# Kernel tuning notes

Hardware: AMD Instinct MI355X
Metric: run time of the kernel (lower is better)

The kernel has to match this reference:

```python
import jax, jax.numpy as jnp
import numpy as np

B, S, D = 2, 2048, 1024
H, DK, DV = 16, 64, 64
DFF = 4096
EPS_RMS = 1e-6


def setup_inputs() -> dict:
    key = jax.random.key(0)
    ks = jax.random.split(key, 10)
    sc = 0.02
    return {
        "x": jax.random.normal(ks[0], (B, S, D), jnp.float32),
        "w_q": jax.random.normal(ks[1], (D, H * DK), jnp.float32) * sc,
        "w_k": jax.random.normal(ks[2], (D, H * DK), jnp.float32) * sc,
        "w_v": jax.random.normal(ks[3], (D, H * DV), jnp.float32) * sc,
        "w_o": jax.random.normal(ks[4], (H * DV, D), jnp.float32) * sc,
        "w_gate": jax.random.normal(ks[5], (D, DFF), jnp.float32) * sc,
        "w_up": jax.random.normal(ks[6], (D, DFF), jnp.float32) * sc,
        "w_down": jax.random.normal(ks[7], (DFF, D), jnp.float32) * sc,
        "g1": jnp.ones((D,), jnp.float32),
        "g2": jnp.ones((D,), jnp.float32),
    }


def _rmsnorm(x, g):
    var = jnp.mean(jnp.square(x), axis=-1, keepdims=True)
    return x * jax.lax.rsqrt(var + EPS_RMS) * g


def _stable_softmax(s):
    # Faithful to source: exp(x) / (sum exp(x) + 1e-9); fully-masked rows -> 0.
    e = jnp.exp(s)
    return e / (jnp.sum(e, axis=-1, keepdims=True) + 1e-9)


def reference(x, w_q, w_k, w_v, w_o, w_gate, w_up, w_down, g1, g2):
    b, s, d = x.shape
    h = _rmsnorm(x, g1)
    q = (h @ w_q).reshape(b, s, H, DK).transpose(0, 2, 1, 3)  # [B,H,S,DK]
    k = (h @ w_k).reshape(b, s, H, DK).transpose(0, 2, 1, 3)
    v = (h @ w_v).reshape(b, s, H, DV).transpose(0, 2, 1, 3)
    scores = jnp.einsum("bhqd,bhkd->bhqk", q, k) / jnp.sqrt(jnp.asarray(DK, x.dtype))
    # triu with diagonal=0: self and future positions are masked
    mask = jnp.triu(jnp.ones((s, s), bool))
    scores = jnp.where(mask, -jnp.inf, scores)
    attn = _stable_softmax(scores)  # [B,H,S,S]
    av = jnp.einsum("bhqk,bhkd->bhqd", attn, v)
    av = av.transpose(0, 2, 1, 3).reshape(b, s, H * DV)
    x = x + av @ w_o  # residual 1
    h2 = _rmsnorm(x, g2)
    hidden = jax.nn.silu(h2 @ w_gate) * (h2 @ w_up)
    return x + hidden @ w_down  # residual 2
```

## Files before the change

### kernel.cpp

```cpp
#include <hip/hip_runtime.h>
#include <cstdint>
#include <cstddef>

typedef unsigned short u16;
typedef unsigned int u32;
typedef __bf16 bf16x8 __attribute__((ext_vector_type(8)));
typedef float floatx4 __attribute__((ext_vector_type(4)));
typedef float floatx16 __attribute__((ext_vector_type(16)));

#define B_ 2
#define S_ 2048
#define D_ 1024
#define H_ 16
#define DFF_ 4096
#define BS_ 4096

__device__ __forceinline__ u16 f2bf(float f) {
  u32 u = __builtin_bit_cast(u32, f);
  u += 0x7fffu + ((u >> 16) & 1u);
  return (u16)(u >> 16);
}
__device__ __forceinline__ float bf2f(u16 h) {
  u32 u = ((u32)h) << 16;
  return __builtin_bit_cast(float, u);
}

__device__ __forceinline__ void gl_lds16(const u16* g, u16* l) {
  __builtin_amdgcn_global_load_lds(
      (const __attribute__((address_space(1))) void*)g,
      (__attribute__((address_space(3))) void*)l, 16, 0, 0);
}

__global__ void prep_weights(const float* __restrict__ wq, const float* __restrict__ wk,
                             const float* __restrict__ wv, const float* __restrict__ wo,
                             const float* __restrict__ wg, const float* __restrict__ wu,
                             const float* __restrict__ wd,
                             u16* __restrict__ wqkv_t, u16* __restrict__ wo_t,
                             u16* __restrict__ wgu_t, u16* __restrict__ wdn_t) {
  __shared__ float tile[32][33];
  const int id = blockIdx.x;
  const float* src;
  u16* dst;
  int R, C, bx, by, mode;
  if (id < 3072) {
    const int which = id >> 10, lo = id & 1023;
    src = which == 0 ? wq : (which == 1 ? wk : wv);
    dst = wqkv_t + which * 1024 * 1024;
    R = 1024; C = 1024; bx = lo & 31; by = lo >> 5; mode = 0;
  } else if (id < 4096) {
    const int lo = id - 3072;
    src = wo; dst = wo_t; R = 1024; C = 1024; bx = lo & 31; by = lo >> 5; mode = 0;
  } else if (id < 8192) {
    const int lo = id - 4096;
    src = wg; dst = wgu_t; R = 1024; C = 4096; bx = lo & 127; by = lo >> 7; mode = 1;
  } else if (id < 12288) {
    const int lo = id - 8192;
    src = wu; dst = wgu_t; R = 1024; C = 4096; bx = lo & 127; by = lo >> 7; mode = 2;
  } else {
    const int lo = id - 12288;
    src = wd; dst = wdn_t; R = 4096; C = 1024; bx = lo & 31; by = lo >> 5; mode = 0;
  }
  const int tx = threadIdx.x, ty = threadIdx.y;
  const int c0 = bx * 32, r0 = by * 32;
#pragma unroll
  for (int i = 0; i < 4; i++)
    tile[ty + i * 8][tx] = src[(size_t)(r0 + ty + i * 8) * C + c0 + tx];
  __syncthreads();
#pragma unroll
  for (int i = 0; i < 4; i++) {
    const int oc = c0 + ty + i * 8;
    const int orow = (mode == 0) ? oc
                                 : ((oc >> 5) * 64 + (oc & 31) + (mode == 2 ? 32 : 0));
    dst[(size_t)orow * R + r0 + tx] = f2bf(tile[tx][ty + i * 8]);
  }
}

__global__ __launch_bounds__(256) void rmsnorm_kernel(const float* __restrict__ x,
                                                      const float* __restrict__ g,
                                                      u16* __restrict__ out) {
  const int row = blockIdx.x, t = threadIdx.x;
  const float4 v = ((const float4*)(x + (size_t)row * 1024))[t];
  float ss = v.x * v.x + v.y * v.y + v.z * v.z + v.w * v.w;
#pragma unroll
  for (int off = 32; off > 0; off >>= 1) ss += __shfl_xor(ss, off);
  __shared__ float red[4];
  if ((t & 63) == 0) red[t >> 6] = ss;
  __syncthreads();
  ss = red[0] + red[1] + red[2] + red[3];
  const float inv = rsqrtf(ss * (1.0f / 1024.0f) + 1e-6f);
  const float4 gv = ((const float4*)g)[t];
  uint2 o;
  o.x = (u32)f2bf(v.x * inv * gv.x) | ((u32)f2bf(v.y * inv * gv.y) << 16);
  o.y = (u32)f2bf(v.z * inv * gv.z) | ((u32)f2bf(v.w * inv * gv.w) << 16);
  ((uint2*)(out + (size_t)row * 1024))[t] = o;
}

__global__ __launch_bounds__(256) void vtrans_kernel(const u16* __restrict__ qkv,
                                                     u16* __restrict__ vT) {
  __shared__ u16 tile[64][72];
  const int t = threadIdx.x;
  const int s0 = blockIdx.x * 64, h = blockIdx.y, b = blockIdx.z;
  const int r = t >> 2, cc = t & 3;
  const u16* src = qkv + (size_t)(b * S_ + s0 + r) * 3072 + 2 * D_ + h * 64 + cc * 16;
  *(uint4*)(&tile[r][cc * 16]) = *(const uint4*)src;
  *(uint4*)(&tile[r][cc * 16 + 8]) = *(const uint4*)(src + 8);
  __syncthreads();
  union { uint4 u[2]; u16 s[16]; } o;
#pragma unroll
  for (int j = 0; j < 16; j++) o.s[j] = tile[cc * 16 + j][r];
  u16* dst = vT + (size_t)((b * H_ + h) * 64 + r) * S_ + s0 + cc * 16;
  *(uint4*)dst = o.u[0];
  *(uint4*)(dst + 8) = o.u[1];
}

template <int BN, int EPI>
__global__ __launch_bounds__(256) void gemm_bt(const u16* __restrict__ A,
                                               const u16* __restrict__ Bt,
                                               void* __restrict__ Cout,
                                               const float* __restrict__ res,
                                               int M, int N, int K) {
  __shared__ u16 As[128 * 64];
  __shared__ u16 Bs[BN * 64];
  constexpr int NTI = BN / 64;
  constexpr int NSEG = 16 + BN / 8;
  constexpr int SPW = NSEG / 4;
  const int t = threadIdx.x, w = t >> 6, l = t & 63;
  const int m0 = blockIdx.y * 128, n0 = blockIdx.x * BN;
  const int wm = w >> 1, wn = w & 1;
  const int c31 = l & 31, khalf = l >> 5;

  const u16* gsrc[SPW];
  u16* ldst[SPW];
  {
    const int rl = l >> 3, ch = (l & 7) ^ rl;
#pragma unroll
    for (int i = 0; i < SPW; i++) {
      const int s = w * SPW + i;
      if (s < 16) {
        gsrc[i] = A + (size_t)(m0 + s * 8 + rl) * K + ch * 8;
        ldst[i] = As + s * 512;
      } else {
        gsrc[i] = Bt + (size_t)(n0 + (s - 16) * 8 + rl) * K + ch * 8;
        ldst[i] = Bs + (s - 16) * 512;
      }
    }
  }

  floatx16 acc[2][NTI] = {};

  for (int kk = 0; kk < K; kk += 64) {
    __syncthreads();
#pragma unroll
    for (int i = 0; i < SPW; i++) gl_lds16(gsrc[i], ldst[i]);
#pragma unroll
    for (int i = 0; i < SPW; i++) gsrc[i] += 64;
    __syncthreads();

#pragma unroll
    for (int ks = 0; ks < 4; ks++) {
      bf16x8 af[2], bfr[NTI];
#pragma unroll
      for (int mi = 0; mi < 2; mi++) {
        const int row = wm * 64 + mi * 32 + c31;
        const int e = (ks * 2 + khalf) ^ (row & 7);
        af[mi] = *(const bf16x8*)(As + row * 64 + e * 8);
      }
#pragma unroll
      for (int ni = 0; ni < NTI; ni++) {
        const int row = wn * (BN / 2) + ni * 32 + c31;
        const int e = (ks * 2 + khalf) ^ (row & 7);
        bfr[ni] = *(const bf16x8*)(Bs + row * 64 + e * 8);
      }
#pragma unroll
      for (int mi = 0; mi < 2; mi++)
#pragma unroll
        for (int ni = 0; ni < NTI; ni++)
          acc[mi][ni] = __builtin_amdgcn_mfma_f32_32x32x16_bf16(af[mi], bfr[ni],
                                                                acc[mi][ni], 0, 0, 0);
    }
  }

  if (EPI == 2) {
#pragma unroll
    for (int mi = 0; mi < 2; mi++) {
      const int colo = ((int)blockIdx.x * 2 + wn) * 32 + c31;
#pragma unroll
      for (int reg = 0; reg < 16; reg++) {
        const int row = m0 + wm * 64 + mi * 32 + (reg & 3) + 8 * (reg >> 2) + 4 * khalf;
        const float g = acc[mi][0][reg];
        const float u = acc[mi][1][reg];
        ((u16*)Cout)[(size_t)row * 4096 + colo] = f2bf(g / (1.f + __expf(-g)) * u);
      }
    }
  } else {
#pragma unroll
    for (int mi = 0; mi < 2; mi++)
#pragma unroll
      for (int ni = 0; ni < NTI; ni++) {
        const int col = n0 + wn * (BN / 2) + ni * 32 + c31;
#pragma unroll
        for (int reg = 0; reg < 16; reg++) {
          const int row = m0 + wm * 64 + mi * 32 + (reg & 3) + 8 * (reg >> 2) + 4 * khalf;
          const size_t idx = (size_t)row * N + col;
          if (EPI == 0) ((u16*)Cout)[idx] = f2bf(acc[mi][ni][reg]);
          else          ((float*)Cout)[idx] = acc[mi][ni][reg] + res[idx];
        }
      }
  }
}

__global__ __launch_bounds__(256) void attn_kernel(const u16* __restrict__ qkv,
                                                   const u16* __restrict__ vT,
                                                   u16* __restrict__ av) {
  __shared__ u16 SM[2 * 8192];
  __shared__ u16 Ps[4 * 2048];
  const int t = threadIdx.x, w = t >> 6, l = t & 63;
  const int lrow = l & 15, lk = l >> 4;
  const int bh = blockIdx.x;
  const int b = bh >> 4, h = bh & 15;
  const int qt = 15 - (int)blockIdx.y;
  const int qbase = qt * 128 + w * 32;
  const int ktmax = 2 * qt + 1;
  u16* Pw = Ps + w * 2048;

  bf16x8 aq[2][2];
#pragma unroll
  for (int sub = 0; sub < 2; sub++)
#pragma unroll
    for (int half = 0; half < 2; half++)
      aq[sub][half] = *(const bf16x8*)(qkv + (size_t)(b * S_ + qbase + sub * 16 + lrow) * 3072 +
                                       h * 64 + half * 32 + lk * 8);

  const u16* gcur[4];
  int gstep[4], loff[4];
#pragma unroll
  for (int i = 0; i < 4; i++) {
    const int c = w + 4 * i;
    const int half = (c >> 2) & 1, grp = c & 3;
    if (c < 8) {
      gcur[i] = qkv + (size_t)(b * S_ + grp * 16 + (l >> 2)) * 3072 + D_ + h * 64 +
                half * 32 + (l & 3) * 8;
      gstep[i] = 64 * 3072;
      loff[i] = half * 2048 + grp * 512;
    } else {
      gcur[i] = vT + (size_t)(bh * 64 + grp * 16 + (l >> 2)) * S_ + half * 32 + (l & 3) * 8;
      gstep[i] = 64;
      loff[i] = 4096 + half * 2048 + grp * 512;
    }
  }

  floatx4 oacc[2][4] = {};
  float den[2][4] = {};

  int cur = 0;
#pragma unroll
  for (int i = 0; i < 4; i++) { gl_lds16(gcur[i], SM + loff[i]); gcur[i] += gstep[i]; }

  for (int kt = 0; kt <= ktmax; kt++) {
    __syncthreads();
    if (kt < ktmax) {
#pragma unroll
      for (int i = 0; i < 4; i++) {
        gl_lds16(gcur[i], SM + (cur ^ 1) * 8192 + loff[i]);
        gcur[i] += gstep[i];
      }
    }
    const u16* Kbuf = SM + cur * 8192;
    const u16* Vbuf = Kbuf + 4096;

    bf16x8 bk[4][2];
#pragma unroll
    for (int ct = 0; ct < 4; ct++)
#pragma unroll
      for (int half = 0; half < 2; half++)
        bk[ct][half] = *(const bf16x8*)(Kbuf + half * 2048 + (ct * 16 + lrow) * 32 + lk * 8);
    floatx4 sf[2][4] = {};
#pragma unroll
    for (int sub = 0; sub < 2; sub++)
#pragma unroll
      for (int ct = 0; ct < 4; ct++) {
        sf[sub][ct] = __builtin_amdgcn_mfma_f32_16x16x32_bf16(aq[sub][0], bk[ct][0],
                                                              sf[sub][ct], 0, 0, 0);
        sf[sub][ct] = __builtin_amdgcn_mfma_f32_16x16x32_bf16(aq[sub][1], bk[ct][1],
                                                              sf[sub][ct], 0, 0, 0);
      }

#pragma unroll
    for (int sub = 0; sub < 2; sub++)
#pragma unroll
      for (int ct = 0; ct < 4; ct++) {
        const int kpos = kt * 64 + ct * 16 + lrow;
#pragma unroll
        for (int r = 0; r < 4; r++) {
          const int qpos = qbase + sub * 16 + lk * 4 + r;
          const float p = (kpos < qpos) ? __expf(sf[sub][ct][r] * 0.125f) : 0.f;
          den[sub][r] += p;
          const int prow = sub * 16 + lk * 4 + r;
          const int pcol = ct * 16 + lrow;
          Pw[prow * 64 + ((((pcol >> 3) ^ (prow & 7))) << 3) + (pcol & 7)] = f2bf(p);
        }
      }

    bf16x8 ap[2][2], bv[4][2];
#pragma unroll
    for (int sub = 0; sub < 2; sub++)
#pragma unroll
      for (int kh = 0; kh < 2; kh++) {
        const int prow = sub * 16 + lrow;
        ap[sub][kh] = *(const bf16x8*)(Pw + prow * 64 + (((kh * 4 + lk) ^ (prow & 7)) << 3));
      }
#pragma unroll
    for (int ni = 0; ni < 4; ni++)
#pragma unroll
      for (int kh = 0; kh < 2; kh++)
        bv[ni][kh] = *(const bf16x8*)(Vbuf + kh * 2048 + (ni * 16 + lrow) * 32 + lk * 8);
#pragma unroll
    for (int sub = 0; sub < 2; sub++)
#pragma unroll
      for (int ni = 0; ni < 4; ni++) {
        oacc[sub][ni] = __builtin_amdgcn_mfma_f32_16x16x32_bf16(ap[sub][0], bv[ni][0],
                                                                oacc[sub][ni], 0, 0, 0);
        oacc[sub][ni] = __builtin_amdgcn_mfma_f32_16x16x32_bf16(ap[sub][1], bv[ni][1],
                                                                oacc[sub][ni], 0, 0, 0);
      }
    cur ^= 1;
  }

#pragma unroll
  for (int sub = 0; sub < 2; sub++)
#pragma unroll
    for (int r = 0; r < 4; r++) {
      float d = den[sub][r];
      d += __shfl_xor(d, 1);
      d += __shfl_xor(d, 2);
      d += __shfl_xor(d, 4);
      d += __shfl_xor(d, 8);
      den[sub][r] = d;
    }
#pragma unroll
  for (int sub = 0; sub < 2; sub++)
#pragma unroll
    for (int ni = 0; ni < 4; ni++)
#pragma unroll
      for (int r = 0; r < 4; r++) {
        const int row = qbase + sub * 16 + lk * 4 + r;
        const int col = h * 64 + ni * 16 + lrow;
        av[(size_t)(b * S_ + row) * 1024 + col] = f2bf(oacc[sub][ni][r] / (den[sub][r] + 1e-9f));
      }
}

#define OFF_WQKV 0u
#define OFF_WO   6291456u
#define OFF_WGU  8388608u
#define OFF_WDN  25165824u
#define OFF_H1   33554432u
#define OFF_QKV  41943040u
#define OFF_VT   67108864u
#define OFF_AV   75497472u
#define OFF_X1   83886080u
#define OFF_H2   100663296u
#define OFF_HID  109051904u

extern "C" void kernel_launch(void* const* d_in, const int* in_sizes, int n_in,
                              void* d_out, int out_size, void* d_ws, size_t ws_size,
                              hipStream_t stream) {
  const float* x      = (const float*)d_in[0];
  const float* w_q    = (const float*)d_in[1];
  const float* w_k    = (const float*)d_in[2];
  const float* w_v    = (const float*)d_in[3];
  const float* w_o    = (const float*)d_in[4];
  const float* w_gate = (const float*)d_in[5];
  const float* w_up   = (const float*)d_in[6];
  const float* w_down = (const float*)d_in[7];
  const float* g1     = (const float*)d_in[8];
  const float* g2     = (const float*)d_in[9];

  char* ws = (char*)d_ws;
  u16* wqkv_t = (u16*)(ws + OFF_WQKV);
  u16* wo_t   = (u16*)(ws + OFF_WO);
  u16* wgu_t  = (u16*)(ws + OFF_WGU);
  u16* wdn_t  = (u16*)(ws + OFF_WDN);
  u16* h1     = (u16*)(ws + OFF_H1);
  u16* qkv    = (u16*)(ws + OFF_QKV);
  u16* vT     = (u16*)(ws + OFF_VT);
  u16* av     = (u16*)(ws + OFF_AV);
  float* x1   = (float*)(ws + OFF_X1);
  u16* h2     = (u16*)(ws + OFF_H2);
  u16* hid    = (u16*)(ws + OFF_HID);
  float* out  = (float*)d_out;

  prep_weights<<<16384, dim3(32, 8), 0, stream>>>(w_q, w_k, w_v, w_o, w_gate, w_up, w_down,
                                                  wqkv_t, wo_t, wgu_t, wdn_t);

  rmsnorm_kernel<<<BS_, 256, 0, stream>>>(x, g1, h1);
  gemm_bt<128, 0><<<dim3(3072 / 128, BS_ / 128), 256, 0, stream>>>(h1, wqkv_t, qkv, nullptr,
                                                                   BS_, 3072, 1024);
  vtrans_kernel<<<dim3(S_ / 64, H_, B_), 256, 0, stream>>>(qkv, vT);
  attn_kernel<<<dim3(32, 16), 256, 0, stream>>>(qkv, vT, av);
  gemm_bt<64, 1><<<dim3(1024 / 64, BS_ / 128), 256, 0, stream>>>(av, wo_t, x1, x,
                                                                 BS_, 1024, 1024);
  rmsnorm_kernel<<<BS_, 256, 0, stream>>>(x1, g2, h2);
  gemm_bt<128, 2><<<dim3(8192 / 128, BS_ / 128), 256, 0, stream>>>(h2, wgu_t, hid, nullptr,
                                                                   BS_, 8192, 1024);
  gemm_bt<64, 1><<<dim3(1024 / 64, BS_ / 128), 256, 0, stream>>>(hid, wdn_t, out, x1,
                                                                 BS_, 1024, 4096);
}
```

Measured before the change: 387.4 us.

## Store GEMM operands in MFMA fragment layout and load directly to registers

Weights, normalized activations, attention output and the SwiGLU hidden tensor are now written in a blocked 32x16 fragment-major layout. The GEMM can then load MFMA operands straight from global memory into registers with contiguous 16-byte loads, skipping LDS staging and the paired block barriers. A two-stage register double buffer overlaps loads with MFMAs. The cost is no LDS reuse across waves, so each wave fetches its own A and B fragments and global/L2 traffic goes up. Register pressure also rises.

```diff
diff --git a/kernel.cpp b/kernel.cpp
--- a/kernel.cpp
+++ b/kernel.cpp
@@ -30,6 +30,7 @@
       (const __attribute__((address_space(1))) void*)g,
       (__attribute__((address_space(3))) void*)l, 16, 0, 0);
 }
+
 
 __global__ void prep_weights(const float* __restrict__ wq, const float* __restrict__ wk,
                              const float* __restrict__ wv, const float* __restrict__ wo,
@@ -41,24 +42,24 @@
   const int id = blockIdx.x;
   const float* src;
   u16* dst;
-  int R, C, bx, by, mode;
+  int R, C, bx, by, mode, KC;
   if (id < 3072) {
     const int which = id >> 10, lo = id & 1023;
     src = which == 0 ? wq : (which == 1 ? wk : wv);
     dst = wqkv_t + which * 1024 * 1024;
-    R = 1024; C = 1024; bx = lo & 31; by = lo >> 5; mode = 0;
+    R = 1024; C = 1024; bx = lo & 31; by = lo >> 5; mode = 0; KC = 64;
   } else if (id < 4096) {
     const int lo = id - 3072;
-    src = wo; dst = wo_t; R = 1024; C = 1024; bx = lo & 31; by = lo >> 5; mode = 0;
+    src = wo; dst = wo_t; R = 1024; C = 1024; bx = lo & 31; by = lo >> 5; mode = 0; KC = 64;
   } else if (id < 8192) {
     const int lo = id - 4096;
-    src = wg; dst = wgu_t; R = 1024; C = 4096; bx = lo & 127; by = lo >> 7; mode = 1;
+    src = wg; dst = wgu_t; R = 1024; C = 4096; bx = lo & 127; by = lo >> 7; mode = 1; KC = 64;
   } else if (id < 12288) {
     const int lo = id - 8192;
-    src = wu; dst = wgu_t; R = 1024; C = 4096; bx = lo & 127; by = lo >> 7; mode = 2;
+    src = wu; dst = wgu_t; R = 1024; C = 4096; bx = lo & 127; by = lo >> 7; mode = 2; KC = 64;
   } else {
     const int lo = id - 12288;
-    src = wd; dst = wdn_t; R = 4096; C = 1024; bx = lo & 31; by = lo >> 5; mode = 0;
+    src = wd; dst = wdn_t; R = 4096; C = 1024; bx = lo & 31; by = lo >> 5; mode = 0; KC = 256;
   }
   const int tx = threadIdx.x, ty = threadIdx.y;
   const int c0 = bx * 32, r0 = by * 32;
@@ -69,9 +70,11 @@
 #pragma unroll
   for (int i = 0; i < 4; i++) {
     const int oc = c0 + ty + i * 8;
-    const int orow = (mode == 0) ? oc
-                                 : ((oc >> 5) * 64 + (oc & 31) + (mode == 2 ? 32 : 0));
-    dst[(size_t)orow * R + r0 + tx] = f2bf(tile[tx][ty + i * 8]);
+    const int nb = (mode == 0) ? (oc >> 5) : ((oc >> 5) * 2 + (mode == 2 ? 1 : 0));
+    const int kc = (r0 >> 4) + (tx >> 4);
+    const size_t addr = ((size_t)nb * KC + kc) * 512 +
+                        ((oc & 31) + 32 * ((tx >> 3) & 1)) * 8 + (tx & 7);
+    dst[addr] = f2bf(tile[tx][ty + i * 8]);
   }
 }
 
@@ -92,7 +95,9 @@
   uint2 o;
   o.x = (u32)f2bf(v.x * inv * gv.x) | ((u32)f2bf(v.y * inv * gv.y) << 16);
   o.y = (u32)f2bf(v.z * inv * gv.z) | ((u32)f2bf(v.w * inv * gv.w) << 16);
-  ((uint2*)(out + (size_t)row * 1024))[t] = o;
+  u16* dst = out + ((size_t)(row >> 5) * 64 + (t >> 2)) * 512 +
+             ((row & 31) + 32 * ((t >> 1) & 1)) * 8 + (t & 1) * 4;
+  *(uint2*)dst = o;
 }
 
 __global__ __launch_bounds__(256) void vtrans_kernel(const u16* __restrict__ qkv,
@@ -114,82 +119,78 @@
 }
 
 template <int BN, int EPI>
-__global__ __launch_bounds__(256) void gemm_bt(const u16* __restrict__ A,
-                                               const u16* __restrict__ Bt,
+__global__ __launch_bounds__(256) void gemm_rf(const u16* __restrict__ Af,
+                                               const u16* __restrict__ Bf,
                                                void* __restrict__ Cout,
                                                const float* __restrict__ res,
                                                int M, int N, int K) {
-  __shared__ u16 As[128 * 64];
-  __shared__ u16 Bs[BN * 64];
   constexpr int NTI = BN / 64;
-  constexpr int NSEG = 16 + BN / 8;
-  constexpr int SPW = NSEG / 4;
   const int t = threadIdx.x, w = t >> 6, l = t & 63;
+  const int wm = w >> 1, wn = w & 1;
   const int m0 = blockIdx.y * 128, n0 = blockIdx.x * BN;
-  const int wm = w >> 1, wn = w & 1;
   const int c31 = l & 31, khalf = l >> 5;
-
-  const u16* gsrc[SPW];
-  u16* ldst[SPW];
-  {
-    const int rl = l >> 3, ch = (l & 7) ^ rl;
-#pragma unroll
-    for (int i = 0; i < SPW; i++) {
-      const int s = w * SPW + i;
-      if (s < 16) {
-        gsrc[i] = A + (size_t)(m0 + s * 8 + rl) * K + ch * 8;
-        ldst[i] = As + s * 512;
-      } else {
-        gsrc[i] = Bt + (size_t)(n0 + (s - 16) * 8 + rl) * K + ch * 8;
-        ldst[i] = Bs + (s - 16) * 512;
-      }
-    }
-  }
+  const int KC = K >> 4;
+
+  const u16* aP[2];
+  const u16* bP[NTI];
+#pragma unroll
+  for (int mi = 0; mi < 2; mi++)
+    aP[mi] = Af + ((size_t)((m0 >> 5) + wm * 2 + mi) * KC) * 512 + l * 8;
+#pragma unroll
+  for (int ni = 0; ni < NTI; ni++)
+    bP[ni] = Bf + ((size_t)((n0 >> 5) + wn * NTI + ni) * KC) * 512 + l * 8;
 
   floatx16 acc[2][NTI] = {};
-
-  for (int kk = 0; kk < K; kk += 64) {
-    __syncthreads();
-#pragma unroll
-    for (int i = 0; i < SPW; i++) gl_lds16(gsrc[i], ldst[i]);
-#pragma unroll
-    for (int i = 0; i < SPW; i++) gsrc[i] += 64;
-    __syncthreads();
-
-#pragma unroll
-    for (int ks = 0; ks < 4; ks++) {
-      bf16x8 af[2], bfr[NTI];
-#pragma unroll
-      for (int mi = 0; mi < 2; mi++) {
-        const int row = wm * 64 + mi * 32 + c31;
-        const int e = (ks * 2 + khalf) ^ (row & 7);
-        af[mi] = *(const bf16x8*)(As + row * 64 + e * 8);
-      }
-#pragma unroll
-      for (int ni = 0; ni < NTI; ni++) {
-        const int row = wn * (BN / 2) + ni * 32 + c31;
-        const int e = (ks * 2 + khalf) ^ (row & 7);
-        bfr[ni] = *(const bf16x8*)(Bs + row * 64 + e * 8);
-      }
-#pragma unroll
-      for (int mi = 0; mi < 2; mi++)
-#pragma unroll
-        for (int ni = 0; ni < NTI; ni++)
-          acc[mi][ni] = __builtin_amdgcn_mfma_f32_32x32x16_bf16(af[mi], bfr[ni],
-                                                                acc[mi][ni], 0, 0, 0);
-    }
-  }
+  bf16x8 a0[2][4], b0[NTI][4], a1[2][4], b1[NTI][4];
+
+#define LD(ab, bb)                                                         \
+  {                                                                        \
+    _Pragma("unroll") for (int mi = 0; mi < 2; mi++)                       \
+        _Pragma("unroll") for (int u = 0; u < 4; u++)                      \
+            ab[mi][u] = *(const bf16x8*)(aP[mi] + u * 512);                \
+    _Pragma("unroll") for (int ni = 0; ni < NTI; ni++)                     \
+        _Pragma("unroll") for (int u = 0; u < 4; u++)                      \
+            bb[ni][u] = *(const bf16x8*)(bP[ni] + u * 512);                \
+    _Pragma("unroll") for (int mi = 0; mi < 2; mi++) aP[mi] += 2048;       \
+    _Pragma("unroll") for (int ni = 0; ni < NTI; ni++) bP[ni] += 2048;     \
+  }
+#define FM(ab, bb)                                                         \
+  {                                                                        \
+    _Pragma("unroll") for (int u = 0; u < 4; u++)                          \
+        _Pragma("unroll") for (int mi = 0; mi < 2; mi++)                   \
+            _Pragma("unroll") for (int ni = 0; ni < NTI; ni++)             \
+                acc[mi][ni] = __builtin_amdgcn_mfma_f32_32x32x16_bf16(     \
+                    ab[mi][u], bb[ni][u], acc[mi][ni], 0, 0, 0);           \
+  }
+
+  LD(a0, b0);
+  const int NIT = K / 64;
+  for (int it = 0; it < NIT - 2; it += 2) {
+    LD(a1, b1);
+    FM(a0, b0);
+    __builtin_amdgcn_s_barrier();
+    LD(a0, b0);
+    FM(a1, b1);
+  }
+  LD(a1, b1);
+  FM(a0, b0);
+  FM(a1, b1);
+#undef LD
+#undef FM
 
   if (EPI == 2) {
+    const int colb = (int)blockIdx.x * 2 + wn;
 #pragma unroll
     for (int mi = 0; mi < 2; mi++) {
-      const int colo = ((int)blockIdx.x * 2 + wn) * 32 + c31;
+      u16* outp = (u16*)Cout +
+                  (((size_t)((m0 >> 5) + wm * 2 + mi) * 256 + colb * 2 + (c31 >> 4)) * 512 +
+                   32 * ((c31 >> 3) & 1) * 8 + (c31 & 7));
 #pragma unroll
       for (int reg = 0; reg < 16; reg++) {
-        const int row = m0 + wm * 64 + mi * 32 + (reg & 3) + 8 * (reg >> 2) + 4 * khalf;
+        const int mir = (reg & 3) + 8 * (reg >> 2) + 4 * khalf;
         const float g = acc[mi][0][reg];
         const float u = acc[mi][1][reg];
-        ((u16*)Cout)[(size_t)row * 4096 + colo] = f2bf(g / (1.f + __expf(-g)) * u);
+        outp[(size_t)mir * 8] = f2bf(g / (1.f + __expf(-g)) * u);
       }
     }
   } else {
@@ -197,7 +198,7 @@
     for (int mi = 0; mi < 2; mi++)
 #pragma unroll
       for (int ni = 0; ni < NTI; ni++) {
-        const int col = n0 + wn * (BN / 2) + ni * 32 + c31;
+        const int col = n0 + (wn * NTI + ni) * 32 + c31;
 #pragma unroll
         for (int reg = 0; reg < 16; reg++) {
           const int row = m0 + wm * 64 + mi * 32 + (reg & 3) + 8 * (reg >> 2) + 4 * khalf;
@@ -343,9 +344,10 @@
     for (int ni = 0; ni < 4; ni++)
 #pragma unroll
       for (int r = 0; r < 4; r++) {
-        const int row = qbase + sub * 16 + lk * 4 + r;
-        const int col = h * 64 + ni * 16 + lrow;
-        av[(size_t)(b * S_ + row) * 1024 + col] = f2bf(oacc[sub][ni][r] / (den[sub][r] + 1e-9f));
+        const int rowl = sub * 16 + lk * 4 + r;
+        const size_t addr = ((size_t)(b * 64 + qt * 4 + w) * 64 + h * 4 + ni) * 512 +
+                            (rowl + 32 * (lrow >> 3)) * 8 + (lrow & 7);
+        av[addr] = f2bf(oacc[sub][ni][r] / (den[sub][r] + 1e-9f));
       }
 }
 
@@ -393,15 +395,15 @@
                                                   wqkv_t, wo_t, wgu_t, wdn_t);
 
   rmsnorm_kernel<<<BS_, 256, 0, stream>>>(x, g1, h1);
-  gemm_bt<128, 0><<<dim3(3072 / 128, BS_ / 128), 256, 0, stream>>>(h1, wqkv_t, qkv, nullptr,
+  gemm_rf<128, 0><<<dim3(3072 / 128, BS_ / 128), 256, 0, stream>>>(h1, wqkv_t, qkv, nullptr,
                                                                    BS_, 3072, 1024);
   vtrans_kernel<<<dim3(S_ / 64, H_, B_), 256, 0, stream>>>(qkv, vT);
   attn_kernel<<<dim3(32, 16), 256, 0, stream>>>(qkv, vT, av);
-  gemm_bt<64, 1><<<dim3(1024 / 64, BS_ / 128), 256, 0, stream>>>(av, wo_t, x1, x,
+  gemm_rf<64, 1><<<dim3(1024 / 64, BS_ / 128), 256, 0, stream>>>(av, wo_t, x1, x,
                                                                  BS_, 1024, 1024);
   rmsnorm_kernel<<<BS_, 256, 0, stream>>>(x1, g2, h2);
-  gemm_bt<128, 2><<<dim3(8192 / 128, BS_ / 128), 256, 0, stream>>>(h2, wgu_t, hid, nullptr,
+  gemm_rf<128, 2><<<dim3(8192 / 128, BS_ / 128), 256, 0, stream>>>(h2, wgu_t, hid, nullptr,
                                                                    BS_, 8192, 1024);
-  gemm_bt<64, 1><<<dim3(1024 / 64, BS_ / 128), 256, 0, stream>>>(hid, wdn_t, out, x1,
+  gemm_rf<64, 1><<<dim3(1024 / 64, BS_ / 128), 256, 0, stream>>>(hid, wdn_t, out, x1,
                                                                  BS_, 1024, 4096);
 }
```

Result: slower. 430.9 us (+11.2%).
